# Kernel optimization log

Measured on AMD Instinct MI355X. Metric: run time of the kernel, lower is better.

## Reference

```python
import jax, jax.numpy as jnp
import numpy as np


def setup_inputs() -> dict:
    key = jax.random.key(0)
    k1, k2 = jax.random.split(key)
    pred = jax.random.normal(k1, (16, 4096, 3), dtype=jnp.float32)
    target = jax.random.normal(k2, (16, 4096, 3), dtype=jnp.float32)
    return {"pred": pred, "target": target}


def _pairwise_l2(pc1, pc2):
    # pc1: (B,N,3), pc2: (B,M,3) -> (B,N,M) euclidean distances (torch.cdist p=2)
    sq1 = jnp.sum(pc1 * pc1, axis=-1)  # (B,N)
    sq2 = jnp.sum(pc2 * pc2, axis=-1)  # (B,M)
    inner = jnp.einsum("bnd,bmd->bnm", pc1, pc2)  # (B,N,M)
    d2 = sq1[:, :, None] + sq2[:, None, :] - 2.0 * inner
    return jnp.sqrt(jnp.maximum(d2, 0.0))


def reference(pred, target):
    d = _pairwise_l2(pred, target)          # (B,N,M)
    dist1 = jnp.mean(jnp.min(d, axis=2), axis=1)  # (B,) pred -> target
    dist2 = jnp.mean(jnp.min(d, axis=1), axis=1)  # (B,) target -> pred
    chamfer = (dist1 + dist2) / 2.0         # bidirectional=True
    return jnp.mean(chamfer)
```

## Files before the change

kernel.cpp:

```cpp
#include <hip/hip_runtime.h>
#include <math.h>
#include <stdint.h>


#define BATCH   16
#define NPTS    4096
#define THREADS 512
#define NITEMS  (2 * BATCH * NPTS)
#define MAIN_BLOCKS (2 * BATCH * (NPTS / 128))

typedef __attribute__((ext_vector_type(8)))  _Float16 half8;
typedef __attribute__((ext_vector_type(16))) float    floatx16;

union Pack16 { float4 f4; _Float16 h[8]; half8 h8; };

__global__ __launch_bounds__(256) void chamfer_prep(
    const float* __restrict__ pred, const float* __restrict__ target,
    float4* __restrict__ packP, float4* __restrict__ packT)
{
    int g = blockIdx.x * 256 + threadIdx.x;
    int arr = g >> 16;
    int pt  = g & 65535;
    const float* src = arr ? target : pred;
    float x = src[pt * 3 + 0];
    float y = src[pt * 3 + 1];
    float z = src[pt * 3 + 2];
    _Float16 hx = (_Float16)x, hy = (_Float16)y, hz = (_Float16)z;
    float xf = (float)hx, yf = (float)hy, zf = (float)hz;
    float t = xf * xf + yf * yf + zf * zf;
    _Float16 h1 = (_Float16)t;
    _Float16 h2 = (_Float16)(t - (float)h1);
    Pack16 p;
    p.h[0] = hx; p.h[1] = hy; p.h[2] = hz; p.h[3] = h1; p.h[4] = h2;
    p.h[5] = (_Float16)0.0f; p.h[6] = (_Float16)0.0f; p.h[7] = (_Float16)0.0f;
    (arr ? packT : packP)[pt] = p.f4;
}

__global__ __launch_bounds__(THREADS, 6) void chamfer_main(
    const float4* __restrict__ packP, const float4* __restrict__ packT,
    float* __restrict__ blocksum)
{
    __shared__ float pmin[8][32];
    __shared__ float wsum[4];

    int tid  = threadIdx.x;
    int lane = tid & 63;
    int wave = tid >> 6;
    int qsub = wave & 3;
    int half = wave >> 2;
    int l31  = lane & 31;
    bool lo  = lane < 32;

    int id = blockIdx.x;
    int ng = id & 31; id >>= 5;
    int b  = id & 15; id >>= 4;
    int dir = id;

    const float4* qpack = dir ? packT : packP;
    const float4* cpack = dir ? packP : packT;

    Pack16 praw;
    praw.f4 = qpack[(size_t)b * NPTS + ng * 128 + qsub * 32 + l31];
    float psq = (float)praw.h[3] + (float)praw.h[4];

    half8 bfrag;
#pragma unroll
    for (int i = 0; i < 8; ++i) bfrag[i] = (_Float16)0.0f;
    if (lo) {
        bfrag[0] = (_Float16)(praw.h[0] * (_Float16)-2.0f);
        bfrag[1] = (_Float16)(praw.h[1] * (_Float16)-2.0f);
        bfrag[2] = (_Float16)(praw.h[2] * (_Float16)-2.0f);
        bfrag[3] = (_Float16)1.0f;
        bfrag[4] = (_Float16)1.0f;
    }

    const float4* cb = cpack + (size_t)b * NPTS + half * 2048;

    floatx16 zero, mn;
#pragma unroll
    for (int r = 0; r < 16; ++r) { zero[r] = 0.0f; mn[r] = 1e30f; }

#pragma unroll 4
    for (int t = 0; t < 32; ++t) {
        Pack16 a0, a1;
        a0.f4 = cb[t * 64 + l31];
        a1.f4 = cb[t * 64 + 32 + l31];
        floatx16 d0 = __builtin_amdgcn_mfma_f32_32x32x16_f16(a0.h8, bfrag, zero, 0, 0, 0);
        floatx16 d1 = __builtin_amdgcn_mfma_f32_32x32x16_f16(a1.h8, bfrag, zero, 0, 0, 0);
#pragma unroll
        for (int r = 0; r < 16; ++r)
            mn[r] = fminf(fminf(d0[r], d1[r]), mn[r]);
    }

    float m0 = fminf(fminf(mn[0], mn[1]),   fminf(mn[2], mn[3]));
    float m1 = fminf(fminf(mn[4], mn[5]),   fminf(mn[6], mn[7]));
    float m2 = fminf(fminf(mn[8], mn[9]),   fminf(mn[10], mn[11]));
    float m3 = fminf(fminf(mn[12], mn[13]), fminf(mn[14], mn[15]));
    float m  = fminf(fminf(m0, m1), fminf(m2, m3));
    m = fminf(m, __shfl_xor(m, 32));
    if (lo) pmin[wave][l31] = m;
    __syncthreads();

    if (wave < 4) {
        float mm = fminf(m, pmin[wave + 4][l31]);
        float dist = sqrtf(fmaxf(mm + psq, 0.0f));
#pragma unroll
        for (int off = 1; off <= 16; off <<= 1)
            dist += __shfl_xor(dist, off);
        if (lane == 0) wsum[wave] = dist;
    }
    __syncthreads();

    if (tid == 0)
        blocksum[blockIdx.x] = wsum[0] + wsum[1] + wsum[2] + wsum[3];
}

__global__ __launch_bounds__(256) void chamfer_finish(
    const float4* __restrict__ bs, float* __restrict__ out)
{
    __shared__ float ws[4];
    int tid = threadIdx.x;
    float4 v = bs[tid];
    float s = v.x + v.y + v.z + v.w;
#pragma unroll
    for (int off = 1; off <= 32; off <<= 1)
        s += __shfl_xor(s, off);
    int lane = tid & 63, wave = tid >> 6;
    if (lane == 0) ws[wave] = s;
    __syncthreads();
    if (tid == 0) out[0] = (ws[0] + ws[1] + ws[2] + ws[3]) * (1.0f / (float)NITEMS);
}

extern "C" void kernel_launch(void* const* d_in, const int* in_sizes, int n_in,
                              void* d_out, int out_size, void* d_ws, size_t ws_size,
                              hipStream_t stream) {
    const float* pred   = (const float*)d_in[0];
    const float* target = (const float*)d_in[1];
    float* out = (float*)d_out;

    float4* packP = (float4*)d_ws;
    float4* packT = packP + (size_t)BATCH * NPTS;
    float*  blocksum = (float*)(packT + (size_t)BATCH * NPTS);

    chamfer_prep<<<NITEMS / 256, 256, 0, stream>>>(pred, target, packP, packT);
    chamfer_main<<<MAIN_BLOCKS, THREADS, 0, stream>>>(packP, packT, blocksum);
    chamfer_finish<<<1, 256, 0, stream>>>((const float4*)blocksum, out);
}
```

Before: 80.68 us.

## Process two query tiles per wave to reuse candidate loads across MFMAs

Halves the block to 4 waves, with each wave now covering 64 query points (two B fragments) against half the candidate set. Every candidate fragment load feeds two MFMAs, so global/L2 loads per MFMA drop by half and fewer waves share the same work. The cost is more accumulator registers per wave (two 16-element min vectors), lower occupancy bound (4 blocks per launch bound), and fewer waves available to hide latency.

```diff
diff --git a/kernel.cpp b/kernel.cpp
--- a/kernel.cpp
+++ b/kernel.cpp
@@ -5,7 +5,7 @@
 
 #define BATCH   16
 #define NPTS    4096
-#define THREADS 512
+#define THREADS 256
 #define NITEMS  (2 * BATCH * NPTS)
 #define MAIN_BLOCKS (2 * BATCH * (NPTS / 128))
 
@@ -36,18 +36,32 @@
     (arr ? packT : packP)[pt] = p.f4;
 }
 
-__global__ __launch_bounds__(THREADS, 6) void chamfer_main(
+__device__ inline half8 make_bfrag(const Pack16& praw, bool lo) {
+    half8 f;
+#pragma unroll
+    for (int i = 0; i < 8; ++i) f[i] = (_Float16)0.0f;
+    if (lo) {
+        f[0] = (_Float16)(praw.h[0] * (_Float16)-2.0f);
+        f[1] = (_Float16)(praw.h[1] * (_Float16)-2.0f);
+        f[2] = (_Float16)(praw.h[2] * (_Float16)-2.0f);
+        f[3] = (_Float16)1.0f;
+        f[4] = (_Float16)1.0f;
+    }
+    return f;
+}
+
+__global__ __launch_bounds__(THREADS, 4) void chamfer_main(
     const float4* __restrict__ packP, const float4* __restrict__ packT,
     float* __restrict__ blocksum)
 {
-    __shared__ float pmin[8][32];
-    __shared__ float wsum[4];
+    __shared__ float pmin[4][64];
+    __shared__ float wsum[2];
 
     int tid  = threadIdx.x;
     int lane = tid & 63;
     int wave = tid >> 6;
-    int qsub = wave & 3;
-    int half = wave >> 2;
+    int qhalf = wave & 1;
+    int chalf = wave >> 1;
     int l31  = lane & 31;
     bool lo  = lane < 32;
 
@@ -59,60 +73,69 @@
     const float4* qpack = dir ? packT : packP;
     const float4* cpack = dir ? packP : packT;
 
-    Pack16 praw;
-    praw.f4 = qpack[(size_t)b * NPTS + ng * 128 + qsub * 32 + l31];
-    float psq = (float)praw.h[3] + (float)praw.h[4];
+    size_t qbase = (size_t)b * NPTS + ng * 128 + qhalf * 64;
+    Pack16 prA, prB;
+    prA.f4 = qpack[qbase + l31];
+    prB.f4 = qpack[qbase + 32 + l31];
+    half8 bfragA = make_bfrag(prA, lo);
+    half8 bfragB = make_bfrag(prB, lo);
 
-    half8 bfrag;
+    const float4* cb = cpack + (size_t)b * NPTS + chalf * 2048;
+
+    floatx16 zero, mnA, mnB;
 #pragma unroll
-    for (int i = 0; i < 8; ++i) bfrag[i] = (_Float16)0.0f;
-    if (lo) {
-        bfrag[0] = (_Float16)(praw.h[0] * (_Float16)-2.0f);
-        bfrag[1] = (_Float16)(praw.h[1] * (_Float16)-2.0f);
-        bfrag[2] = (_Float16)(praw.h[2] * (_Float16)-2.0f);
-        bfrag[3] = (_Float16)1.0f;
-        bfrag[4] = (_Float16)1.0f;
-    }
+    for (int r = 0; r < 16; ++r) { zero[r] = 0.0f; mnA[r] = 1e30f; mnB[r] = 1e30f; }
 
-    const float4* cb = cpack + (size_t)b * NPTS + half * 2048;
-
-    floatx16 zero, mn;
-#pragma unroll
-    for (int r = 0; r < 16; ++r) { zero[r] = 0.0f; mn[r] = 1e30f; }
-
-#pragma unroll 4
+#pragma unroll 2
     for (int t = 0; t < 32; ++t) {
         Pack16 a0, a1;
         a0.f4 = cb[t * 64 + l31];
         a1.f4 = cb[t * 64 + 32 + l31];
-        floatx16 d0 = __builtin_amdgcn_mfma_f32_32x32x16_f16(a0.h8, bfrag, zero, 0, 0, 0);
-        floatx16 d1 = __builtin_amdgcn_mfma_f32_32x32x16_f16(a1.h8, bfrag, zero, 0, 0, 0);
+        floatx16 d0 = __builtin_amdgcn_mfma_f32_32x32x16_f16(a0.h8, bfragA, zero, 0, 0, 0);
+        floatx16 d1 = __builtin_amdgcn_mfma_f32_32x32x16_f16(a0.h8, bfragB, zero, 0, 0, 0);
 #pragma unroll
-        for (int r = 0; r < 16; ++r)
-            mn[r] = fminf(fminf(d0[r], d1[r]), mn[r]);
+        for (int r = 0; r < 16; ++r) mnA[r] = fminf(d0[r], mnA[r]);
+#pragma unroll
+        for (int r = 0; r < 16; ++r) mnB[r] = fminf(d1[r], mnB[r]);
+        floatx16 d2 = __builtin_amdgcn_mfma_f32_32x32x16_f16(a1.h8, bfragA, zero, 0, 0, 0);
+        floatx16 d3 = __builtin_amdgcn_mfma_f32_32x32x16_f16(a1.h8, bfragB, zero, 0, 0, 0);
+#pragma unroll
+        for (int r = 0; r < 16; ++r) mnA[r] = fminf(d2[r], mnA[r]);
+#pragma unroll
+        for (int r = 0; r < 16; ++r) mnB[r] = fminf(d3[r], mnB[r]);
     }
 
-    float m0 = fminf(fminf(mn[0], mn[1]),   fminf(mn[2], mn[3]));
-    float m1 = fminf(fminf(mn[4], mn[5]),   fminf(mn[6], mn[7]));
-    float m2 = fminf(fminf(mn[8], mn[9]),   fminf(mn[10], mn[11]));
-    float m3 = fminf(fminf(mn[12], mn[13]), fminf(mn[14], mn[15]));
-    float m  = fminf(fminf(m0, m1), fminf(m2, m3));
-    m = fminf(m, __shfl_xor(m, 32));
-    if (lo) pmin[wave][l31] = m;
+    float mA = fminf(fminf(fminf(mnA[0], mnA[1]),   fminf(mnA[2], mnA[3])),
+                     fminf(fminf(mnA[4], mnA[5]),   fminf(mnA[6], mnA[7])));
+    mA = fminf(mA, fminf(fminf(fminf(mnA[8], mnA[9]),   fminf(mnA[10], mnA[11])),
+                         fminf(fminf(mnA[12], mnA[13]), fminf(mnA[14], mnA[15]))));
+    float mB = fminf(fminf(fminf(mnB[0], mnB[1]),   fminf(mnB[2], mnB[3])),
+                     fminf(fminf(mnB[4], mnB[5]),   fminf(mnB[6], mnB[7])));
+    mB = fminf(mB, fminf(fminf(fminf(mnB[8], mnB[9]),   fminf(mnB[10], mnB[11])),
+                         fminf(fminf(mnB[12], mnB[13]), fminf(mnB[14], mnB[15]))));
+    mA = fminf(mA, __shfl_xor(mA, 32));
+    mB = fminf(mB, __shfl_xor(mB, 32));
+    if (lo) {
+        pmin[wave][l31]      = mA;
+        pmin[wave][l31 + 32] = mB;
+    }
     __syncthreads();
 
-    if (wave < 4) {
-        float mm = fminf(m, pmin[wave + 4][l31]);
+    if (wave < 2) {
+        float mm = fminf(pmin[wave][lane], pmin[wave + 2][lane]);
+        Pack16 pr;
+        pr.f4 = qpack[(size_t)b * NPTS + ng * 128 + wave * 64 + lane];
+        float psq = (float)pr.h[3] + (float)pr.h[4];
         float dist = sqrtf(fmaxf(mm + psq, 0.0f));
 #pragma unroll
-        for (int off = 1; off <= 16; off <<= 1)
+        for (int off = 1; off <= 32; off <<= 1)
             dist += __shfl_xor(dist, off);
         if (lane == 0) wsum[wave] = dist;
     }
     __syncthreads();
 
     if (tid == 0)
-        blocksum[blockIdx.x] = wsum[0] + wsum[1] + wsum[2] + wsum[3];
+        blocksum[blockIdx.x] = wsum[0] + wsum[1];
 }
 
 __global__ __launch_bounds__(256) void chamfer_finish(
@@ -121,7 +144,7 @@
     __shared__ float ws[4];
     int tid = threadIdx.x;
     float4 v = bs[tid];
-    float s = v.x + v.y + v.z + v.w;
+    float s = (v.x + v.y) + (v.z + v.w);
 #pragma unroll
     for (int off = 1; off <= 32; off <<= 1)
         s += __shfl_xor(s, off);
```

Measured after the change: 76.02 us (median of 2 runs). 1.06x faster.
